# Kernel tuning notes

Measured on AMD Instinct MI355X. Metric: run time of the kernel, lower is better.

The kernel has to match this reference:

```python
import jax, jax.numpy as jnp
import numpy as np

N = 8192
D = 768
TEMPERATURE = 0.1
EPS_NORM = 1e-8   # torch CosineSimilarity eps
EPS_LOG = 1e-6


def setup_inputs() -> dict:
    key = jax.random.key(0)
    k1, k2, k3 = jax.random.split(key, 3)
    features = jax.random.normal(k1, (N, D), dtype=jnp.float32)
    positive_mask = jax.random.randint(k2, (N, N), 0, 2).astype(jnp.float32)
    negative_mask = jax.random.randint(k3, (N, N), 0, 2).astype(jnp.float32)
    return {"features": features, "positive_mask": positive_mask, "negative_mask": negative_mask}


def reference(features, positive_mask, negative_mask):
    n = features.shape[0]
    # cosine similarity: normalize then GEMM (same math as broadcasted CosineSimilarity)
    norms = jnp.linalg.norm(features, axis=1, keepdims=True)
    fn = features / jnp.maximum(norms, EPS_NORM)
    sim = jnp.exp(jnp.matmul(fn, fn.T) / TEMPERATURE)  # [N, N]
    # zero out self-contrast on the diagonal of both masks
    not_eye = 1.0 - jnp.eye(n, dtype=features.dtype)
    pm = positive_mask * not_eye
    nm = negative_mask * not_eye
    pos_sums = pm.sum(axis=1)
    pos_sums = jnp.where(pos_sums == 0, 1.0, pos_sums)
    neg = jnp.sum(sim * nm, axis=1, keepdims=True)  # [N, 1]
    log_prob = -jnp.log(sim / neg + EPS_LOG)        # [N, N]
    per_row = jnp.sum(log_prob * pm, axis=1) / pos_sums
    return jnp.mean(per_row)
```

## Files before the change

### kernel.cpp

```cpp
#include <hip/hip_runtime.h>
#include <hip/hip_bf16.h>

#define NROWS 8192
#define DDIM 768

typedef short short8 __attribute__((ext_vector_type(8)));
typedef float floatx4 __attribute__((ext_vector_type(4)));
#define TSTRIDE 132

__global__ __launch_bounds__(256) void normalize_k(const float* __restrict__ f,
                                                   __hip_bfloat16* __restrict__ fn) {
    const int row = blockIdx.x;
    const int t = threadIdx.x;
    const float* fr = f + (size_t)row * DDIM;
    float v0 = fr[t];
    float v1 = fr[t + 256];
    float v2 = fr[t + 512];
    float ss = v0 * v0 + v1 * v1 + v2 * v2;
#pragma unroll
    for (int m = 32; m; m >>= 1) ss += __shfl_xor(ss, m, 64);
    __shared__ float wsum[4];
    if ((t & 63) == 0) wsum[t >> 6] = ss;
    __syncthreads();
    float tot = wsum[0] + wsum[1] + wsum[2] + wsum[3];
    float inv = 1.0f / fmaxf(sqrtf(tot), 1e-8f);
    __hip_bfloat16* o = fn + (size_t)row * DDIM;
    o[t]       = __float2bfloat16(v0 * inv);
    o[t + 256] = __float2bfloat16(v1 * inv);
    o[t + 512] = __float2bfloat16(v2 * inv);
}

__global__ __launch_bounds__(256, 4) void ntxent_main(
        const __hip_bfloat16* __restrict__ fn,
        const float* __restrict__ pmask, const float* __restrict__ nmask,
        float* __restrict__ negG, float* __restrict__ sG,
        float* __restrict__ pG) {
    __shared__ __align__(16) char smem[32 * TSTRIDE * 4];
    __hip_bfloat16* Is = (__hip_bfloat16*)smem;
    __hip_bfloat16* Js = Is + 128 * 32;
    float* T = (float*)smem;

    const int t = threadIdx.x;
    const int lane = t & 63;
    const int wv = t >> 6;
    const int wm = wv & 1;
    const int wn = wv >> 1;
    const int q  = lane >> 4;
    const int cl = lane & 15;

    const int bt = blockIdx.x;
    int r = (int)((sqrtf(8.0f * (float)bt + 1.0f) - 1.0f) * 0.5f);
    while ((r + 1) * (r + 2) / 2 <= bt) ++r;
    while (r * (r + 1) / 2 > bt) --r;
    const int c = bt - r * (r + 1) / 2;
    const int rowBase = c * 128;
    const int colBase = r * 128;
    const bool offDiag = (c != r);

    const int rdSw = ((q ^ ((cl >> 1) & 3)) << 4);

    floatx4 acc[4][4];
#pragma unroll
    for (int mf = 0; mf < 4; ++mf)
#pragma unroll
        for (int nf = 0; nf < 4; ++nf)
            acc[mf][nf] = (floatx4){0.f, 0.f, 0.f, 0.f};

    for (int k0 = 0; k0 < DDIM; k0 += 32) {
        __syncthreads();
#pragma unroll
        for (int it = 0; it < 2; ++it) {
            const int s = it * 256 + t;
            const int rr = s >> 2;
            const int cg = (s & 3) ^ ((rr >> 1) & 3);
            const __hip_bfloat16* ga = fn + (size_t)(rowBase + rr) * DDIM + k0 + cg * 8;
            const __hip_bfloat16* gb = fn + (size_t)(colBase + rr) * DDIM + k0 + cg * 8;
            __builtin_amdgcn_global_load_lds(
                (const __attribute__((address_space(1))) void*)ga,
                (__attribute__((address_space(3))) void*)((char*)Is + s * 16), 16, 0, 0);
            __builtin_amdgcn_global_load_lds(
                (const __attribute__((address_space(1))) void*)gb,
                (__attribute__((address_space(3))) void*)((char*)Js + s * 16), 16, 0, 0);
        }
        __syncthreads();

        short8 jf[4], if_[4];
#pragma unroll
        for (int mf = 0; mf < 4; ++mf) {
            const int rr = wm * 64 + mf * 16 + cl;
            jf[mf] = *(const short8*)((const char*)Js + rr * 64 + rdSw);
        }
#pragma unroll
        for (int nf = 0; nf < 4; ++nf) {
            const int rr = wn * 64 + nf * 16 + cl;
            if_[nf] = *(const short8*)((const char*)Is + rr * 64 + rdSw);
        }
#pragma unroll
        for (int mf = 0; mf < 4; ++mf)
#pragma unroll
            for (int nf = 0; nf < 4; ++nf)
                acc[mf][nf] = __builtin_amdgcn_mfma_f32_16x16x32_bf16(
                    jf[mf], if_[nf], acc[mf][nf], 0, 0, 0);
    }

    const int col64 = colBase + wm * 64;
    const int jb0 = col64 + q * 4;
#pragma unroll
    for (int nf = 0; nf < 4; ++nf) {
        const int grow = rowBase + wn * 64 + nf * 16 + cl;
        const float* prow = pmask + (size_t)grow * NROWS;
        const float* nrow = nmask + (size_t)grow * NROWS;
        float4 pm4[4], nm4[4];
#pragma unroll
        for (int mf = 0; mf < 4; ++mf) {
            pm4[mf] = *(const float4*)(prow + jb0 + mf * 16);
            nm4[mf] = *(const float4*)(nrow + jb0 + mf * 16);
        }
        float aN = 0.f, aS = 0.f, aP = 0.f;
#pragma unroll
        for (int mf = 0; mf < 4; ++mf) {
            const int jbase = jb0 + mf * 16;
#pragma unroll
            for (int reg = 0; reg < 4; ++reg) {
                float pmv = ((const float*)&pm4[mf])[reg];
                float nmv = ((const float*)&nm4[mf])[reg];
                if (grow == jbase + reg) { pmv = 0.f; nmv = 0.f; }
                float v = acc[mf][nf][reg];
                float e = __builtin_amdgcn_exp2f(v * 14.4269504089f);
                aN = fmaf(nmv, e, aN);
                aS = fmaf(pmv, v, aS);
                aP += pmv;
            }
        }
        aN += __shfl_xor(aN, 16, 64);  aN += __shfl_xor(aN, 32, 64);
        aS += __shfl_xor(aS, 16, 64);  aS += __shfl_xor(aS, 32, 64);
        aP += __shfl_xor(aP, 16, 64);  aP += __shfl_xor(aP, 32, 64);
        if (q == 0) {
            atomicAdd(&negG[grow], aN);
            atomicAdd(&sG[grow],   aS);
            atomicAdd(&pG[grow],   aP);
        }
    }

    if (offDiag) {
        const int jl2 = t >> 3;
        const int iseg = (t & 7) * 16;
#pragma unroll
        for (int st = 0; st < 4; ++st) {
            __syncthreads();
            if (wm == (st >> 1)) {
#pragma unroll
                for (int m2 = 0; m2 < 2; ++m2) {
                    const int mf = (st & 1) * 2 + m2;
#pragma unroll
                    for (int nf = 0; nf < 4; ++nf) {
                        const int i = wn * 64 + nf * 16 + cl;
#pragma unroll
                        for (int reg = 0; reg < 4; ++reg) {
                            const int jl = m2 * 16 + q * 4 + reg;
                            T[jl * TSTRIDE + i] = acc[mf][nf][reg];
                        }
                    }
                }
            }
            __syncthreads();
            const int jg = colBase + st * 32 + jl2;
            const float* prow = pmask + (size_t)jg * NROWS + rowBase + iseg;
            const float* nrow = nmask + (size_t)jg * NROWS + rowBase + iseg;
            float4 pm4[4], nm4[4];
#pragma unroll
            for (int u = 0; u < 4; ++u) {
                pm4[u] = *(const float4*)(prow + u * 4);
                nm4[u] = *(const float4*)(nrow + u * 4);
            }
            const float4* tv = (const float4*)(T + jl2 * TSTRIDE + iseg);
            float aN = 0.f, aS = 0.f, aP = 0.f;
#pragma unroll
            for (int u = 0; u < 4; ++u) {
                float4 v4 = tv[u];
#pragma unroll
                for (int e = 0; e < 4; ++e) {
                    float v = ((const float*)&v4)[e];
                    float pmv = ((const float*)&pm4[u])[e];
                    float nmv = ((const float*)&nm4[u])[e];
                    float ex = __builtin_amdgcn_exp2f(v * 14.4269504089f);
                    aN = fmaf(nmv, ex, aN);
                    aS = fmaf(pmv, v, aS);
                    aP += pmv;
                }
            }
            aN += __shfl_xor(aN, 1, 64); aN += __shfl_xor(aN, 2, 64); aN += __shfl_xor(aN, 4, 64);
            aS += __shfl_xor(aS, 1, 64); aS += __shfl_xor(aS, 2, 64); aS += __shfl_xor(aS, 4, 64);
            aP += __shfl_xor(aP, 1, 64); aP += __shfl_xor(aP, 2, 64); aP += __shfl_xor(aP, 4, 64);
            if ((t & 7) == 0) {
                atomicAdd(&negG[jg], aN);
                atomicAdd(&sG[jg],   aS);
                atomicAdd(&pG[jg],   aP);
            }
        }
    }
}

__global__ __launch_bounds__(1024) void final_k(const float* __restrict__ negG,
        const float* __restrict__ sG, const float* __restrict__ pG,
        float* __restrict__ out) {
    const int t = threadIdx.x;
    float sum = 0.f;
    for (int i = t; i < NROWS; i += 1024) {
        float P = pG[i];
        if (P > 0.f) {
            sum += (P * logf(negG[i]) - 10.0f * sG[i]) / P;
        }
    }
#pragma unroll
    for (int m = 32; m; m >>= 1) sum += __shfl_xor(sum, m, 64);
    __shared__ float wsum[16];
    if ((t & 63) == 0) wsum[t >> 6] = sum;
    __syncthreads();
    if (t < 16) {
        float v = wsum[t];
#pragma unroll
        for (int m = 8; m; m >>= 1) v += __shfl_xor(v, m, 16);
        if (t == 0) out[0] = v / (float)NROWS;
    }
}

extern "C" void kernel_launch(void* const* d_in, const int* in_sizes, int n_in,
                              void* d_out, int out_size, void* d_ws, size_t ws_size,
                              hipStream_t stream) {
    const float* feat  = (const float*)d_in[0];
    const float* pmask = (const float*)d_in[1];
    const float* nmask = (const float*)d_in[2];
    float* out = (float*)d_out;

    char* ws = (char*)d_ws;
    __hip_bfloat16* fn = (__hip_bfloat16*)ws;
    float* negG = (float*)(ws + 12582912);
    float* sG = negG + NROWS;
    float* pG = sG + NROWS;

    hipMemsetAsync(negG, 0, 3 * NROWS * sizeof(float), stream);

    normalize_k<<<NROWS, 256, 0, stream>>>(feat, fn);

    ntxent_main<<<2080, 256, 0, stream>>>(fn, pmask, nmask, negG, sG, pG);

    final_k<<<1, 1024, 0, stream>>>(negG, sG, pG, out);
}
```

Measured before the change: 590.6 us.

## Double-buffer K-loop LDS tiles, swizzle block order, use nontemporal mask loads

The GEMM K-loop now uses two LDS buffers, so the next tile's global-to-LDS loads are in flight while MFMAs run on the current tile, synchronised with explicit vmcnt waits and barriers. Block indices are remapped in strides of 8 (likely to spread blocks across XCDs), and the mask reads use nontemporal loads to avoid polluting cache with streamed data. In exchange, shared memory doubles to 32KB, which may cut occupancy, and the hand-written vmcnt count is fragile if the compiler reorders memory operations.

```diff
diff --git a/kernel.cpp b/kernel.cpp
--- a/kernel.cpp
+++ b/kernel.cpp
@@ -6,6 +6,7 @@
 
 typedef short short8 __attribute__((ext_vector_type(8)));
 typedef float floatx4 __attribute__((ext_vector_type(4)));
+typedef float f4 __attribute__((ext_vector_type(4)));
 #define TSTRIDE 132
 
 __global__ __launch_bounds__(256) void normalize_k(const float* __restrict__ f,
@@ -35,9 +36,7 @@
         const float* __restrict__ pmask, const float* __restrict__ nmask,
         float* __restrict__ negG, float* __restrict__ sG,
         float* __restrict__ pG) {
-    __shared__ __align__(16) char smem[32 * TSTRIDE * 4];
-    __hip_bfloat16* Is = (__hip_bfloat16*)smem;
-    __hip_bfloat16* Js = Is + 128 * 32;
+    __shared__ __align__(16) char smem[2 * 16384];
     float* T = (float*)smem;
 
     const int t = threadIdx.x;
@@ -48,7 +47,9 @@
     const int q  = lane >> 4;
     const int cl = lane & 15;
 
-    const int bt = blockIdx.x;
+    const int bt0 = blockIdx.x;
+    const int bt = (bt0 & 7) * 260 + (bt0 >> 3);
+
     int r = (int)((sqrtf(8.0f * (float)bt + 1.0f) - 1.0f) * 0.5f);
     while ((r + 1) * (r + 2) / 2 <= bt) ++r;
     while (r * (r + 1) / 2 > bt) --r;
@@ -66,8 +67,8 @@
         for (int nf = 0; nf < 4; ++nf)
             acc[mf][nf] = (floatx4){0.f, 0.f, 0.f, 0.f};
 
-    for (int k0 = 0; k0 < DDIM; k0 += 32) {
-        __syncthreads();
+    auto stage = [&](int buf, int k0) {
+        char* isb = smem + buf * 16384;
 #pragma unroll
         for (int it = 0; it < 2; ++it) {
             const int s = it * 256 + t;
@@ -77,23 +78,35 @@
             const __hip_bfloat16* gb = fn + (size_t)(colBase + rr) * DDIM + k0 + cg * 8;
             __builtin_amdgcn_global_load_lds(
                 (const __attribute__((address_space(1))) void*)ga,
-                (__attribute__((address_space(3))) void*)((char*)Is + s * 16), 16, 0, 0);
+                (__attribute__((address_space(3))) void*)(isb + s * 16), 16, 0, 0);
             __builtin_amdgcn_global_load_lds(
                 (const __attribute__((address_space(1))) void*)gb,
-                (__attribute__((address_space(3))) void*)((char*)Js + s * 16), 16, 0, 0);
-        }
-        __syncthreads();
-
+                (__attribute__((address_space(3))) void*)(isb + 8192 + s * 16), 16, 0, 0);
+        }
+    };
+
+    stage(0, 0);
+    for (int kt = 0; kt < 24; ++kt) {
+        const int cur = kt & 1;
+        if (kt < 23) {
+            stage(cur ^ 1, (kt + 1) * 32);
+            asm volatile("s_waitcnt vmcnt(4)\n\ts_barrier" ::: "memory");
+        } else {
+            asm volatile("s_waitcnt vmcnt(0)\n\ts_barrier" ::: "memory");
+        }
+
+        const char* IsC = smem + cur * 16384;
+        const char* JsC = IsC + 8192;
         short8 jf[4], if_[4];
 #pragma unroll
         for (int mf = 0; mf < 4; ++mf) {
             const int rr = wm * 64 + mf * 16 + cl;
-            jf[mf] = *(const short8*)((const char*)Js + rr * 64 + rdSw);
+            jf[mf] = *(const short8*)(JsC + rr * 64 + rdSw);
         }
 #pragma unroll
         for (int nf = 0; nf < 4; ++nf) {
             const int rr = wn * 64 + nf * 16 + cl;
-            if_[nf] = *(const short8*)((const char*)Is + rr * 64 + rdSw);
+            if_[nf] = *(const short8*)(IsC + rr * 64 + rdSw);
         }
 #pragma unroll
         for (int mf = 0; mf < 4; ++mf)
@@ -101,6 +114,8 @@
             for (int nf = 0; nf < 4; ++nf)
                 acc[mf][nf] = __builtin_amdgcn_mfma_f32_16x16x32_bf16(
                     jf[mf], if_[nf], acc[mf][nf], 0, 0, 0);
+
+        asm volatile("s_barrier" ::: "memory");
     }
 
     const int col64 = colBase + wm * 64;
@@ -110,11 +125,11 @@
         const int grow = rowBase + wn * 64 + nf * 16 + cl;
         const float* prow = pmask + (size_t)grow * NROWS;
         const float* nrow = nmask + (size_t)grow * NROWS;
-        float4 pm4[4], nm4[4];
+        f4 pm4[4], nm4[4];
 #pragma unroll
         for (int mf = 0; mf < 4; ++mf) {
-            pm4[mf] = *(const float4*)(prow + jb0 + mf * 16);
-            nm4[mf] = *(const float4*)(nrow + jb0 + mf * 16);
+            pm4[mf] = __builtin_nontemporal_load((const f4*)(prow + jb0 + mf * 16));
+            nm4[mf] = __builtin_nontemporal_load((const f4*)(nrow + jb0 + mf * 16));
         }
         float aN = 0.f, aS = 0.f, aP = 0.f;
 #pragma unroll
@@ -122,8 +137,8 @@
             const int jbase = jb0 + mf * 16;
 #pragma unroll
             for (int reg = 0; reg < 4; ++reg) {
-                float pmv = ((const float*)&pm4[mf])[reg];
-                float nmv = ((const float*)&nm4[mf])[reg];
+                float pmv = pm4[mf][reg];
+                float nmv = nm4[mf][reg];
                 if (grow == jbase + reg) { pmv = 0.f; nmv = 0.f; }
                 float v = acc[mf][nf][reg];
                 float e = __builtin_amdgcn_exp2f(v * 14.4269504089f);
@@ -167,22 +182,22 @@
             const int jg = colBase + st * 32 + jl2;
             const float* prow = pmask + (size_t)jg * NROWS + rowBase + iseg;
             const float* nrow = nmask + (size_t)jg * NROWS + rowBase + iseg;
-            float4 pm4[4], nm4[4];
+            f4 pm4[4], nm4[4];
 #pragma unroll
             for (int u = 0; u < 4; ++u) {
-                pm4[u] = *(const float4*)(prow + u * 4);
-                nm4[u] = *(const float4*)(nrow + u * 4);
-            }
-            const float4* tv = (const float4*)(T + jl2 * TSTRIDE + iseg);
+                pm4[u] = __builtin_nontemporal_load((const f4*)(prow + u * 4));
+                nm4[u] = __builtin_nontemporal_load((const f4*)(nrow + u * 4));
+            }
+            const f4* tv = (const f4*)(T + jl2 * TSTRIDE + iseg);
             float aN = 0.f, aS = 0.f, aP = 0.f;
 #pragma unroll
             for (int u = 0; u < 4; ++u) {
-                float4 v4 = tv[u];
+                f4 v4 = tv[u];
 #pragma unroll
                 for (int e = 0; e < 4; ++e) {
-                    float v = ((const float*)&v4)[e];
-                    float pmv = ((const float*)&pm4[u])[e];
-                    float nmv = ((const float*)&nm4[u])[e];
+                    float v = v4[e];
+                    float pmv = pm4[u][e];
+                    float nmv = nm4[u][e];
                     float ex = __builtin_amdgcn_exp2f(v * 14.4269504089f);
                     aN = fmaf(nmv, ex, aN);
                     aS = fmaf(pmv, v, aS);
```

New measurement: 620.0 us. 5.0% more time.

## Prefetch mask tiles into LDS during GEMM k-loop, pack as bitmasks

Applied to the files above, without the earlier changes.

Mask loads for both the direct and mirrored epilogues are spread across the 24 k-iterations using async global-to-LDS loads. Each value is converted to a bit in 64-bit registers, so the epilogue no longer stalls on large mask reads after the GEMM. Block indices are also remapped across 8 groups, which changes tile scheduling and locality. This costs extra LDS space, adds instructions inside the k-loop, and treats mask values as 0/1 by thresholding at 0.5.

```diff
diff --git a/kernel.cpp b/kernel.cpp
--- a/kernel.cpp
+++ b/kernel.cpp
@@ -6,6 +6,7 @@
 
 typedef short short8 __attribute__((ext_vector_type(8)));
 typedef float floatx4 __attribute__((ext_vector_type(4)));
+typedef float f4 __attribute__((ext_vector_type(4)));
 #define TSTRIDE 132
 
 __global__ __launch_bounds__(256) void normalize_k(const float* __restrict__ f,
@@ -35,9 +36,10 @@
         const float* __restrict__ pmask, const float* __restrict__ nmask,
         float* __restrict__ negG, float* __restrict__ sG,
         float* __restrict__ pG) {
-    __shared__ __align__(16) char smem[32 * TSTRIDE * 4];
+    __shared__ __align__(16) char smem[28672];
     __hip_bfloat16* Is = (__hip_bfloat16*)smem;
     __hip_bfloat16* Js = Is + 128 * 32;
+    char* maskLds = smem + 16384;
     float* T = (float*)smem;
 
     const int t = threadIdx.x;
@@ -48,7 +50,9 @@
     const int q  = lane >> 4;
     const int cl = lane & 15;
 
-    const int bt = blockIdx.x;
+    const int bt0 = blockIdx.x;
+    const int bt = (bt0 & 7) * 260 + (bt0 >> 3);
+
     int r = (int)((sqrtf(8.0f * (float)bt + 1.0f) - 1.0f) * 0.5f);
     while ((r + 1) * (r + 2) / 2 <= bt) ++r;
     while (r * (r + 1) / 2 > bt) --r;
@@ -66,8 +70,37 @@
         for (int nf = 0; nf < 4; ++nf)
             acc[mf][nf] = (floatx4){0.f, 0.f, 0.f, 0.f};
 
-    for (int k0 = 0; k0 < DDIM; k0 += 32) {
+    unsigned long long pD = 0ull, nD = 0ull, pM = 0ull, nM = 0ull;
+
+    for (int kt = 0; kt < 24; ++kt) {
+        const int k0 = kt * 32;
         __syncthreads();
+
+#pragma unroll
+        for (int ql = 0; ql < 3; ++ql) {
+            const int qq = kt * 3 + ql;
+            if (qq >= 64) break;
+            const bool mir = (qq >= 32);
+            if (mir && !offDiag) continue;
+            const bool isN = (qq & 1);
+            const float* mp = isN ? nmask : pmask;
+            int row, col;
+            if (!mir) {
+                const int nf = qq >> 3, mf = (qq >> 1) & 3;
+                row = rowBase + wn * 64 + nf * 16 + cl;
+                col = colBase + wm * 64 + q * 4 + mf * 16;
+            } else {
+                const int m2 = qq - 32, st = m2 >> 3, u = (m2 >> 1) & 3;
+                row = colBase + st * 32 + (t >> 3);
+                col = rowBase + (t & 7) * 16 + u * 4;
+            }
+            const float* src = mp + (size_t)row * NROWS + col;
+            __builtin_amdgcn_global_load_lds(
+                (const __attribute__((address_space(1))) void*)src,
+                (__attribute__((address_space(3))) void*)(maskLds + (ql * 256 + t) * 16),
+                16, 0, 0);
+        }
+
 #pragma unroll
         for (int it = 0; it < 2; ++it) {
             const int s = it * 256 + t;
@@ -101,6 +134,24 @@
             for (int nf = 0; nf < 4; ++nf)
                 acc[mf][nf] = __builtin_amdgcn_mfma_f32_16x16x32_bf16(
                     jf[mf], if_[nf], acc[mf][nf], 0, 0, 0);
+
+#pragma unroll
+        for (int ql = 0; ql < 3; ++ql) {
+            const int qq = kt * 3 + ql;
+            if (qq >= 64) break;
+            const bool mir = (qq >= 32);
+            if (mir && !offDiag) continue;
+            const f4 m4 = *(const f4*)(maskLds + (ql * 256 + t) * 16);
+            const int mq = mir ? qq - 32 : qq;
+            const int bb = ((mq >> 3) << 4) | (((mq >> 1) & 3) << 2);
+            unsigned long long add = 0ull;
+#pragma unroll
+            for (int e = 0; e < 4; ++e)
+                add |= (m4[e] > 0.5f) ? (1ull << (bb + e)) : 0ull;
+            const bool isN = (qq & 1);
+            if (!mir) { if (!isN) pD |= add; else nD |= add; }
+            else      { if (!isN) pM |= add; else nM |= add; }
+        }
     }
 
     const int col64 = colBase + wm * 64;
@@ -108,22 +159,15 @@
 #pragma unroll
     for (int nf = 0; nf < 4; ++nf) {
         const int grow = rowBase + wn * 64 + nf * 16 + cl;
-        const float* prow = pmask + (size_t)grow * NROWS;
-        const float* nrow = nmask + (size_t)grow * NROWS;
-        float4 pm4[4], nm4[4];
-#pragma unroll
-        for (int mf = 0; mf < 4; ++mf) {
-            pm4[mf] = *(const float4*)(prow + jb0 + mf * 16);
-            nm4[mf] = *(const float4*)(nrow + jb0 + mf * 16);
-        }
         float aN = 0.f, aS = 0.f, aP = 0.f;
 #pragma unroll
         for (int mf = 0; mf < 4; ++mf) {
             const int jbase = jb0 + mf * 16;
 #pragma unroll
             for (int reg = 0; reg < 4; ++reg) {
-                float pmv = ((const float*)&pm4[mf])[reg];
-                float nmv = ((const float*)&nm4[mf])[reg];
+                const int b = nf * 16 + mf * 4 + reg;
+                float pmv = ((pD >> b) & 1ull) ? 1.0f : 0.0f;
+                float nmv = ((nD >> b) & 1ull) ? 1.0f : 0.0f;
                 if (grow == jbase + reg) { pmv = 0.f; nmv = 0.f; }
                 float v = acc[mf][nf][reg];
                 float e = __builtin_amdgcn_exp2f(v * 14.4269504089f);
@@ -165,24 +209,17 @@
             }
             __syncthreads();
             const int jg = colBase + st * 32 + jl2;
-            const float* prow = pmask + (size_t)jg * NROWS + rowBase + iseg;
-            const float* nrow = nmask + (size_t)jg * NROWS + rowBase + iseg;
-            float4 pm4[4], nm4[4];
+            const f4* tv = (const f4*)(T + jl2 * TSTRIDE + iseg);
+            float aN = 0.f, aS = 0.f, aP = 0.f;
 #pragma unroll
             for (int u = 0; u < 4; ++u) {
-                pm4[u] = *(const float4*)(prow + u * 4);
-                nm4[u] = *(const float4*)(nrow + u * 4);
-            }
-            const float4* tv = (const float4*)(T + jl2 * TSTRIDE + iseg);
-            float aN = 0.f, aS = 0.f, aP = 0.f;
-#pragma unroll
-            for (int u = 0; u < 4; ++u) {
-                float4 v4 = tv[u];
+                f4 v4 = tv[u];
 #pragma unroll
                 for (int e = 0; e < 4; ++e) {
-                    float v = ((const float*)&v4)[e];
-                    float pmv = ((const float*)&pm4[u])[e];
-                    float nmv = ((const float*)&nm4[u])[e];
+                    const int b = st * 16 + u * 4 + e;
+                    float v = v4[e];
+                    float pmv = ((pM >> b) & 1ull) ? 1.0f : 0.0f;
+                    float nmv = ((nM >> b) & 1ull) ? 1.0f : 0.0f;
                     float ex = __builtin_amdgcn_exp2f(v * 14.4269504089f);
                     aN = fmaf(nmv, ex, aN);
                     aS = fmaf(pmv, v, aS);
```

Result: slower. 643.8 us (+9.0%).

## Prefetch mask tiles into LDS during GEMM loop and pack them as bits

Applied to the files above, without the earlier changes.

The positive and negative mask tiles are now streamed asynchronously into a 6-slot LDS ring with global_load_lds, interleaved with the bf16 K-loop. Each slab is packed into per-thread 32-bit words of mask bits, so the epilogue no longer issues large, latency-bound global float4 mask loads after the MFMA work. Block indices are also remapped to change the order of triangular tiles. The cost is more LDS, hand-written waitcnt/barrier sequencing, and an assumption that mask values are exactly 0 or 1.

```diff
diff --git a/kernel.cpp b/kernel.cpp
--- a/kernel.cpp
+++ b/kernel.cpp
@@ -6,6 +6,7 @@
 
 typedef short short8 __attribute__((ext_vector_type(8)));
 typedef float floatx4 __attribute__((ext_vector_type(4)));
+typedef float f4 __attribute__((ext_vector_type(4)));
 #define TSTRIDE 132
 
 __global__ __launch_bounds__(256) void normalize_k(const float* __restrict__ f,
@@ -35,9 +36,10 @@
         const float* __restrict__ pmask, const float* __restrict__ nmask,
         float* __restrict__ negG, float* __restrict__ sG,
         float* __restrict__ pG) {
-    __shared__ __align__(16) char smem[32 * TSTRIDE * 4];
+    __shared__ __align__(16) char smem[40960];
     __hip_bfloat16* Is = (__hip_bfloat16*)smem;
     __hip_bfloat16* Js = Is + 128 * 32;
+    char* maskLds = smem + 16384;
     float* T = (float*)smem;
 
     const int t = threadIdx.x;
@@ -48,7 +50,9 @@
     const int q  = lane >> 4;
     const int cl = lane & 15;
 
-    const int bt = blockIdx.x;
+    const int bt0 = blockIdx.x;
+    const int bt = (bt0 & 7) * 260 + (bt0 >> 3);
+
     int r = (int)((sqrtf(8.0f * (float)bt + 1.0f) - 1.0f) * 0.5f);
     while ((r + 1) * (r + 2) / 2 <= bt) ++r;
     while (r * (r + 1) / 2 > bt) --r;
@@ -59,6 +63,9 @@
 
     const int rdSw = ((q ^ ((cl >> 1) & 3)) << 4);
 
+    const int sRow = t >> 5;
+    const int sChunk = (t & 31) ^ (sRow & 7);
+
     floatx4 acc[4][4];
 #pragma unroll
     for (int mf = 0; mf < 4; ++mf)
@@ -66,8 +73,69 @@
         for (int nf = 0; nf < 4; ++nf)
             acc[mf][nf] = (floatx4){0.f, 0.f, 0.f, 0.f};
 
-    for (int k0 = 0; k0 < DDIM; k0 += 32) {
-        __syncthreads();
+    unsigned int dw[4] = {0u, 0u, 0u, 0u};
+    unsigned int mw[4] = {0u, 0u, 0u, 0u};
+
+    auto issue_slab = [&](int s) {
+        const int slot = s % 6;
+        const int side = s >> 5;
+        const int rg   = (s & 31) >> 1;
+        const float* mp = (s & 1) ? nmask : pmask;
+        const int rowG = (side ? colBase : rowBase) + rg * 8 + sRow;
+        const int colG = (side ? rowBase : colBase) + sChunk * 4;
+        const float* src = mp + (size_t)rowG * NROWS + colG;
+        __builtin_amdgcn_global_load_lds(
+            (const __attribute__((address_space(1))) void*)src,
+            (__attribute__((address_space(3))) void*)(maskLds + slot * 4096 + t * 16),
+            16, 0, 0);
+    };
+
+    auto pack_slab = [&](int s) {
+        const int slot = s % 6;
+        const int side = s >> 5;
+        const int rg   = (s & 31) >> 1;
+        const int sh   = (s & 1) ? 16 : 0;
+        if (side == 0) {
+            if (wn == (rg >> 3) && (cl >> 3) == (rg & 1)) {
+                const int nf = (rg >> 1) & 3;
+                const int rl = cl & 7;
+                const char* base = maskLds + slot * 4096 + rl * 512;
+                float word = 0.f;
+#pragma unroll
+                for (int mf = 3; mf >= 0; --mf) {
+                    const int pos = (wm * 16 + mf * 4 + q) ^ rl;
+                    const f4 m = *(const f4*)(base + pos * 16);
+                    float nib = fmaf(2.f, m[1], m[0]) + fmaf(8.f, m[3], 4.f * m[2]);
+                    word = fmaf(word, 16.f, nib);
+                }
+                dw[nf] |= ((unsigned int)word) << sh;
+            }
+        } else if (offDiag) {
+            if (wv == (rg & 3)) {
+                const int st = rg >> 2;
+                const int rl = (t >> 3) & 7;
+                const int h  = t & 7;
+                const char* base = maskLds + slot * 4096 + rl * 512;
+                float word = 0.f;
+#pragma unroll
+                for (int u = 3; u >= 0; --u) {
+                    const int pos = (h * 4 + u) ^ rl;
+                    const f4 m = *(const f4*)(base + pos * 16);
+                    float nib = fmaf(2.f, m[1], m[0]) + fmaf(8.f, m[3], 4.f * m[2]);
+                    word = fmaf(word, 16.f, nib);
+                }
+                mw[st] |= ((unsigned int)word) << sh;
+            }
+        }
+    };
+
+    issue_slab(0); issue_slab(1); issue_slab(2);
+
+#pragma unroll
+    for (int kt = 0; kt < 24; ++kt) {
+        const int k0 = kt * 32;
+        asm volatile("s_waitcnt lgkmcnt(0)\n\ts_barrier" ::: "memory");
+
 #pragma unroll
         for (int it = 0; it < 2; ++it) {
             const int s = it * 256 + t;
@@ -82,7 +150,16 @@
                 (const __attribute__((address_space(1))) void*)gb,
                 (__attribute__((address_space(3))) void*)((char*)Js + s * 16), 16, 0, 0);
         }
-        __syncthreads();
+
+#pragma unroll
+        for (int gl = 0; gl < 3; ++gl) {
+            const int s = 3 * (kt + 1) + gl;
+            if (s <= 63) issue_slab(s);
+        }
+
+        if (kt < 20)       asm volatile("s_waitcnt vmcnt(3)\n\ts_barrier" ::: "memory");
+        else if (kt == 20) asm volatile("s_waitcnt vmcnt(1)\n\ts_barrier" ::: "memory");
+        else               asm volatile("s_waitcnt vmcnt(0)\n\ts_barrier" ::: "memory");
 
         short8 jf[4], if_[4];
 #pragma unroll
@@ -101,6 +178,12 @@
             for (int nf = 0; nf < 4; ++nf)
                 acc[mf][nf] = __builtin_amdgcn_mfma_f32_16x16x32_bf16(
                     jf[mf], if_[nf], acc[mf][nf], 0, 0, 0);
+
+#pragma unroll
+        for (int gl = 0; gl < 3; ++gl) {
+            const int s = 3 * kt + gl;
+            if (s <= 63) pack_slab(s);
+        }
     }
 
     const int col64 = colBase + wm * 64;
@@ -108,22 +191,16 @@
 #pragma unroll
     for (int nf = 0; nf < 4; ++nf) {
         const int grow = rowBase + wn * 64 + nf * 16 + cl;
-        const float* prow = pmask + (size_t)grow * NROWS;
-        const float* nrow = nmask + (size_t)grow * NROWS;
-        float4 pm4[4], nm4[4];
-#pragma unroll
-        for (int mf = 0; mf < 4; ++mf) {
-            pm4[mf] = *(const float4*)(prow + jb0 + mf * 16);
-            nm4[mf] = *(const float4*)(nrow + jb0 + mf * 16);
-        }
+        const unsigned int w = dw[nf];
         float aN = 0.f, aS = 0.f, aP = 0.f;
 #pragma unroll
         for (int mf = 0; mf < 4; ++mf) {
             const int jbase = jb0 + mf * 16;
 #pragma unroll
             for (int reg = 0; reg < 4; ++reg) {
-                float pmv = ((const float*)&pm4[mf])[reg];
-                float nmv = ((const float*)&nm4[mf])[reg];
+                const int b = mf * 4 + reg;
+                float pmv = ((w >> b) & 1u) ? 1.0f : 0.0f;
+                float nmv = ((w >> (16 + b)) & 1u) ? 1.0f : 0.0f;
                 if (grow == jbase + reg) { pmv = 0.f; nmv = 0.f; }
                 float v = acc[mf][nf][reg];
                 float e = __builtin_amdgcn_exp2f(v * 14.4269504089f);
@@ -165,24 +242,18 @@
             }
             __syncthreads();
             const int jg = colBase + st * 32 + jl2;
-            const float* prow = pmask + (size_t)jg * NROWS + rowBase + iseg;
-            const float* nrow = nmask + (size_t)jg * NROWS + rowBase + iseg;
-            float4 pm4[4], nm4[4];
+            const unsigned int w = mw[st];
+            const f4* tv = (const f4*)(T + jl2 * TSTRIDE + iseg);
+            float aN = 0.f, aS = 0.f, aP = 0.f;
 #pragma unroll
             for (int u = 0; u < 4; ++u) {
-                pm4[u] = *(const float4*)(prow + u * 4);
-                nm4[u] = *(const float4*)(nrow + u * 4);
-            }
-            const float4* tv = (const float4*)(T + jl2 * TSTRIDE + iseg);
-            float aN = 0.f, aS = 0.f, aP = 0.f;
-#pragma unroll
-            for (int u = 0; u < 4; ++u) {
-                float4 v4 = tv[u];
+                f4 v4 = tv[u];
 #pragma unroll
                 for (int e = 0; e < 4; ++e) {
-                    float v = ((const float*)&v4)[e];
-                    float pmv = ((const float*)&pm4[u])[e];
-                    float nmv = ((const float*)&nm4[u])[e];
+                    const int b = u * 4 + e;
+                    float v = v4[e];
+                    float pmv = ((w >> b) & 1u) ? 1.0f : 0.0f;
+                    float nmv = ((w >> (16 + b)) & 1u) ? 1.0f : 0.0f;
                     float ex = __builtin_amdgcn_exp2f(v * 14.4269504089f);
                     aN = fmaf(nmv, ex, aN);
                     aS = fmaf(pmv, v, aS);
```

Result: slower. 646.8 us (+9.5%).
